# Performance work log

Measured on AMD Instinct MI355X. Metric: run time of the kernel, lower is better.

## Reference

```python
import jax, jax.numpy as jnp
import numpy as np

D_MODEL = 1024
NUM_HEADS = 16
HEAD_DIM = D_MODEL // NUM_HEADS
FFN_HIDDEN = 4096
EPS = 1e-5


def setup_inputs() -> dict:
    key = jax.random.key(0)
    ks = jax.random.split(key, 7)
    s = 0.02
    return {
        "x": jax.random.normal(ks[0], (2, 2048, D_MODEL), dtype=jnp.float32),
        "W_qkv": jax.random.normal(ks[1], (D_MODEL, 3 * D_MODEL), dtype=jnp.float32) * s,
        "b_qkv": jnp.zeros((3 * D_MODEL,), dtype=jnp.float32),
        "W_o": jax.random.normal(ks[2], (D_MODEL, D_MODEL), dtype=jnp.float32) * s,
        "b_o": jnp.zeros((D_MODEL,), dtype=jnp.float32),
        "gamma1": jnp.ones((D_MODEL,), dtype=jnp.float32),
        "beta1": jnp.zeros((D_MODEL,), dtype=jnp.float32),
        "W1": jax.random.normal(ks[3], (D_MODEL, FFN_HIDDEN), dtype=jnp.float32) * s,
        "b1": jnp.zeros((FFN_HIDDEN,), dtype=jnp.float32),
        "W2": jax.random.normal(ks[4], (FFN_HIDDEN, D_MODEL), dtype=jnp.float32) * s,
        "b2": jnp.zeros((D_MODEL,), dtype=jnp.float32),
        "gamma2": jnp.ones((D_MODEL,), dtype=jnp.float32),
        "beta2": jnp.zeros((D_MODEL,), dtype=jnp.float32),
    }


def _layernorm(x, gamma, beta):
    mean = jnp.mean(x, axis=-1, keepdims=True)
    var = jnp.mean((x - mean) ** 2, axis=-1, keepdims=True)
    return gamma * (x - mean) / jnp.sqrt(var + EPS) + beta


def reference(x, W_qkv, b_qkv, W_o, b_o, gamma1, beta1, W1, b1, W2, b2, gamma2, beta2):
    B, S, D = x.shape
    # ---- multi-head attention ----
    qkv = x @ W_qkv + b_qkv                       # [B,S,3D]
    qkv = qkv.reshape(B, S, NUM_HEADS, 3 * HEAD_DIM).transpose(0, 2, 1, 3)  # [B,H,S,3hd]
    q, k, v = jnp.split(qkv, 3, axis=-1)          # each [B,H,S,hd]
    scores = jnp.einsum("bhqd,bhkd->bhqk", q, k) / np.sqrt(HEAD_DIM)
    attn = jax.nn.softmax(scores, axis=-1)
    vals = jnp.einsum("bhqk,bhkd->bhqd", attn, v)
    vals = vals.transpose(0, 2, 1, 3).reshape(B, S, D)
    attn_out = vals @ W_o + b_o
    # dropout disabled (eval mode)
    h = _layernorm(attn_out + x, gamma1, beta1)
    # ---- position-wise FFN (dropout before relu per source, disabled) ----
    ffn = jax.nn.relu(h @ W1 + b1) @ W2 + b2
    return _layernorm(ffn + h, gamma2, beta2)
```

## Files before the change

### kernel.cpp

```cpp
#include <hip/hip_runtime.h>
#include <stdint.h>

typedef float v4f __attribute__((ext_vector_type(4)));
typedef __bf16 v8bf __attribute__((ext_vector_type(8)));
typedef __bf16 v4bf __attribute__((ext_vector_type(4)));
typedef unsigned short v8us __attribute__((ext_vector_type(8)));
typedef unsigned short v4us __attribute__((ext_vector_type(4)));

__device__ __forceinline__ float b2f(unsigned short u) {
    union { float f; uint32_t i; } x; x.i = ((uint32_t)u) << 16; return x.f;
}
__device__ __forceinline__ unsigned short f2b(float f) {
    union { float f; uint32_t u; } x; x.f = f;
    uint32_t r = x.u + 0x7fffu + ((x.u >> 16) & 1u);
    return (unsigned short)(r >> 16);
}

__global__ __launch_bounds__(256) void convert_f32_bf16(
    const float* __restrict__ src, unsigned short* __restrict__ dst)
{
    int i = (blockIdx.x * 256 + threadIdx.x) * 4;
    float4 v = *(const float4*)&src[i];
    v4us o = {f2b(v.x), f2b(v.y), f2b(v.z), f2b(v.w)};
    *(v4us*)&dst[i] = o;
}

__global__ __launch_bounds__(256) void transpose_to_bt(
    const float* __restrict__ W, unsigned short* __restrict__ WT, int K, int N)
{
    __shared__ unsigned short t[64][65];
    const int kb = blockIdx.y * 64, nb = blockIdx.x * 64;
    const int r = threadIdx.x >> 4, c4 = (threadIdx.x & 15) * 4;
    #pragma unroll
    for (int i = 0; i < 4; ++i) {
        int k = r + i * 16;
        float4 v = *(const float4*)&W[(size_t)(kb + k) * N + nb + c4];
        t[c4 + 0][k] = f2b(v.x);
        t[c4 + 1][k] = f2b(v.y);
        t[c4 + 2][k] = f2b(v.z);
        t[c4 + 3][k] = f2b(v.w);
    }
    __syncthreads();
    #pragma unroll
    for (int i = 0; i < 4; ++i) {
        int n = r + i * 16;
        v4us o = {t[n][c4], t[n][c4 + 1], t[n][c4 + 2], t[n][c4 + 3]};
        *(v4us*)&WT[(size_t)(nb + n) * K + kb + c4] = o;
    }
}

__device__ __forceinline__ void xcd_swizzle(int& bm, int& bn) {
    int NB = gridDim.x, MB = gridDim.y;
    int flat = blockIdx.x + NB * blockIdx.y;
    int xcd = flat & 7, j = flat >> 3;
    int MBand = MB >> 3;
    bm = xcd * MBand + (j % MBand);
    bn = j / MBand;
}

template<int SPLIT_V>
__global__ __launch_bounds__(256) void gemm_bt(
    const unsigned short* __restrict__ A, const unsigned short* __restrict__ BT,
    const float* __restrict__ bias, unsigned short* __restrict__ C,
    unsigned short* __restrict__ VT, int M, int N, int K, int relu)
{
    __shared__ __align__(16) unsigned short sA[2][128 * 32];
    __shared__ __align__(16) unsigned short sB[2][128 * 32];
    const int tid  = threadIdx.x;
    const int wave = tid >> 6, lane = tid & 63;
    const int wm = wave >> 1, wn = wave & 1;
    const int quad = lane >> 4, l16 = lane & 15;
    int bm, bn;
    xcd_swizzle(bm, bn);

    const int srow = lane >> 2, scol = (lane & 3) * 8;
    const unsigned short* ga0 = A  + (size_t)(bm * 128 + (wave * 2 + 0) * 16 + srow) * K + scol;
    const unsigned short* ga1 = A  + (size_t)(bm * 128 + (wave * 2 + 1) * 16 + srow) * K + scol;
    const unsigned short* gb0 = BT + (size_t)(bn * 128 + (wave * 2 + 0) * 16 + srow) * K + scol;
    const unsigned short* gb1 = BT + (size_t)(bn * 128 + (wave * 2 + 1) * 16 + srow) * K + scol;
    const int o0 = (wave * 2 + 0) * 512 + lane * 8;
    const int o1 = (wave * 2 + 1) * 512 + lane * 8;

    v8us aR[2][2], bR[2][2];
    #pragma unroll
    for (int c = 0; c < 2; ++c) {
        aR[c][0] = *(const v8us*)(ga0 + c * 32);
        aR[c][1] = *(const v8us*)(ga1 + c * 32);
        bR[c][0] = *(const v8us*)(gb0 + c * 32);
        bR[c][1] = *(const v8us*)(gb1 + c * 32);
    }

    v4f acc[4][4];
    #pragma unroll
    for (int i = 0; i < 4; ++i)
        #pragma unroll
        for (int j = 0; j < 4; ++j)
            acc[i][j] = (v4f){0.f, 0.f, 0.f, 0.f};

    for (int kt = 0; kt < K; kt += 64) {
        __syncthreads();
        #pragma unroll
        for (int c = 0; c < 2; ++c) {
            *(v8us*)&sA[c][o0] = aR[c][0];
            *(v8us*)&sA[c][o1] = aR[c][1];
            *(v8us*)&sB[c][o0] = bR[c][0];
            *(v8us*)&sB[c][o1] = bR[c][1];
        }
        __syncthreads();
        if (kt + 64 < K) {
            int kn = kt + 64;
            #pragma unroll
            for (int c = 0; c < 2; ++c) {
                aR[c][0] = *(const v8us*)(ga0 + kn + c * 32);
                aR[c][1] = *(const v8us*)(ga1 + kn + c * 32);
                bR[c][0] = *(const v8us*)(gb0 + kn + c * 32);
                bR[c][1] = *(const v8us*)(gb1 + kn + c * 32);
            }
        }

        #pragma unroll
        for (int c = 0; c < 2; ++c) {
            v8bf af[4], bfr[4];
            #pragma unroll
            for (int mt = 0; mt < 4; ++mt)
                af[mt] = *(const v8bf*)&sA[c][(wm * 64 + mt * 16 + l16) * 32 + quad * 8];
            #pragma unroll
            for (int nt = 0; nt < 4; ++nt)
                bfr[nt] = *(const v8bf*)&sB[c][(wn * 64 + nt * 16 + l16) * 32 + quad * 8];
            #pragma unroll
            for (int mt = 0; mt < 4; ++mt)
                #pragma unroll
                for (int nt = 0; nt < 4; ++nt)
                    acc[mt][nt] = __builtin_amdgcn_mfma_f32_16x16x32_bf16(
                        af[mt], bfr[nt], acc[mt][nt], 0, 0, 0);
        }
    }

    #pragma unroll
    for (int mt = 0; mt < 4; ++mt) {
        int row = bm * 128 + wm * 64 + mt * 16 + quad * 4;
        #pragma unroll
        for (int nt = 0; nt < 4; ++nt) {
            int c0 = bn * 128 + wn * 64 + nt * 16;
            int col = c0 + l16;
            float bv = bias ? bias[col] : 0.f;
            if (SPLIT_V && (c0 % 192) >= 128) {
                int hh = c0 / 192;
                int d  = (c0 % 192) - 128 + l16;
                int bb = row >> 11;
                int s  = row & 2047;
                v4us st;
                #pragma unroll
                for (int r = 0; r < 4; ++r)
                    st[r] = f2b(acc[mt][nt][r] + bv);
                *(v4us*)&VT[((size_t)(bb * 16 + hh) * 64 + d) * 2048 + s] = st;
            } else {
                float qs = (SPLIT_V && (c0 % 192) < 64) ? 0.18033688f : 1.0f;
                #pragma unroll
                for (int r = 0; r < 4; ++r) {
                    float v = (acc[mt][nt][r] + bv) * qs;
                    if (relu) v = fmaxf(v, 0.f);
                    C[(size_t)(row + r) * N + col] = f2b(v);
                }
            }
        }
    }
}

__global__ __launch_bounds__(256) void gemm_bt_n64(
    const unsigned short* __restrict__ A, const unsigned short* __restrict__ BT,
    const float* __restrict__ bias, unsigned short* __restrict__ C,
    int M, int N, int K, int relu)
{
    __shared__ __align__(16) unsigned short sA[2][128 * 32];
    __shared__ __align__(16) unsigned short sB[2][64 * 32];
    const int tid  = threadIdx.x;
    const int wave = tid >> 6, lane = tid & 63;
    const int wm = wave >> 1, wn = wave & 1;
    const int quad = lane >> 4, l16 = lane & 15;
    int bm, bn;
    xcd_swizzle(bm, bn);

    const int srow = lane >> 2, scol = (lane & 3) * 8;
    const unsigned short* ga0 = A  + (size_t)(bm * 128 + (wave * 2 + 0) * 16 + srow) * K + scol;
    const unsigned short* ga1 = A  + (size_t)(bm * 128 + (wave * 2 + 1) * 16 + srow) * K + scol;
    const unsigned short* gb0 = BT + (size_t)(bn * 64 + wave * 16 + srow) * K + scol;
    const int oa0 = (wave * 2 + 0) * 512 + lane * 8;
    const int oa1 = (wave * 2 + 1) * 512 + lane * 8;
    const int ob  = wave * 512 + lane * 8;

    v8us aR[2][2], bR[2];
    #pragma unroll
    for (int c = 0; c < 2; ++c) {
        aR[c][0] = *(const v8us*)(ga0 + c * 32);
        aR[c][1] = *(const v8us*)(ga1 + c * 32);
        bR[c]    = *(const v8us*)(gb0 + c * 32);
    }

    v4f acc[4][2];
    #pragma unroll
    for (int i = 0; i < 4; ++i)
        #pragma unroll
        for (int j = 0; j < 2; ++j)
            acc[i][j] = (v4f){0.f, 0.f, 0.f, 0.f};

    for (int kt = 0; kt < K; kt += 64) {
        __syncthreads();
        #pragma unroll
        for (int c = 0; c < 2; ++c) {
            *(v8us*)&sA[c][oa0] = aR[c][0];
            *(v8us*)&sA[c][oa1] = aR[c][1];
            *(v8us*)&sB[c][ob]  = bR[c];
        }
        __syncthreads();
        if (kt + 64 < K) {
            int kn = kt + 64;
            #pragma unroll
            for (int c = 0; c < 2; ++c) {
                aR[c][0] = *(const v8us*)(ga0 + kn + c * 32);
                aR[c][1] = *(const v8us*)(ga1 + kn + c * 32);
                bR[c]    = *(const v8us*)(gb0 + kn + c * 32);
            }
        }

        #pragma unroll
        for (int c = 0; c < 2; ++c) {
            v8bf af[4], bfr[2];
            #pragma unroll
            for (int mt = 0; mt < 4; ++mt)
                af[mt] = *(const v8bf*)&sA[c][(wm * 64 + mt * 16 + l16) * 32 + quad * 8];
            #pragma unroll
            for (int nt = 0; nt < 2; ++nt)
                bfr[nt] = *(const v8bf*)&sB[c][(wn * 32 + nt * 16 + l16) * 32 + quad * 8];
            #pragma unroll
            for (int mt = 0; mt < 4; ++mt)
                #pragma unroll
                for (int nt = 0; nt < 2; ++nt)
                    acc[mt][nt] = __builtin_amdgcn_mfma_f32_16x16x32_bf16(
                        af[mt], bfr[nt], acc[mt][nt], 0, 0, 0);
        }
    }

    #pragma unroll
    for (int mt = 0; mt < 4; ++mt) {
        #pragma unroll
        for (int nt = 0; nt < 2; ++nt) {
            int col = bn * 64 + wn * 32 + nt * 16 + l16;
            float bv = bias ? bias[col] : 0.f;
            #pragma unroll
            for (int r = 0; r < 4; ++r) {
                int row = bm * 128 + wm * 64 + mt * 16 + quad * 4 + r;
                float v = acc[mt][nt][r] + bv;
                if (relu) v = fmaxf(v, 0.f);
                C[(size_t)row * N + col] = f2b(v);
            }
        }
    }
}

__global__ __launch_bounds__(256) void attn_mfma(
    const unsigned short* __restrict__ qkv, const unsigned short* __restrict__ VT,
    unsigned short* __restrict__ av)
{
    __shared__ __align__(16) unsigned short sK[64 * 72];
    __shared__ __align__(16) unsigned short sVT[64 * 72];
    __shared__ __align__(16) unsigned short sP[4][32 * 72];
    const int tid  = threadIdx.x;
    const int wave = tid >> 6, lane = tid & 63;
    const int quad = lane >> 4, l16 = lane & 15;
    const int blk = blockIdx.x;
    const int xcd = blk & 7, local = blk >> 3;
    const int bh = xcd * 4 + (local & 3);
    const int qb = local >> 2;
    const int h = bh & 15, b = bh >> 4;
    const int row0 = b * 2048;
    const int qbase = row0 + qb * 128 + wave * 32;
    const size_t qoff = (size_t)h * 192;
    const size_t koff = qoff + 64;

    v8bf qf[2][2];
    #pragma unroll
    for (int qt = 0; qt < 2; ++qt)
        #pragma unroll
        for (int kc = 0; kc < 2; ++kc)
            qf[qt][kc] = *(const v8bf*)&qkv[(size_t)(qbase + qt * 16 + l16) * 3072
                                            + qoff + kc * 32 + quad * 8];

    v4f o[4][2];
    #pragma unroll
    for (int dt = 0; dt < 4; ++dt)
        #pragma unroll
        for (int qt = 0; qt < 2; ++qt)
            o[dt][qt] = (v4f){0.f, 0.f, 0.f, 0.f};
    float ll[2] = {0.f, 0.f};

    const int k_key0 = tid >> 3,        k_oct = (tid & 7) * 8;
    const int k_key1 = (tid + 256) >> 3;
    const int v_d0 = tid >> 3,          v_koct = (tid & 7) * 8;
    const int v_d1 = (tid + 256) >> 3;
    const unsigned short* gK0 = qkv + (size_t)(row0 + k_key0) * 3072 + koff + k_oct;
    const unsigned short* gK1 = qkv + (size_t)(row0 + k_key1) * 3072 + koff + k_oct;
    const unsigned short* gV0 = VT + ((size_t)bh * 64 + v_d0) * 2048 + v_koct;
    const unsigned short* gV1 = VT + ((size_t)bh * 64 + v_d1) * 2048 + v_koct;
    const size_t stepK = (size_t)64 * 3072;
    const size_t stepV = 64;

    v8us kreg0 = *(const v8us*)gK0, kreg1 = *(const v8us*)gK1;
    v8us vreg0 = *(const v8us*)gV0, vreg1 = *(const v8us*)gV1;
    gK0 += stepK; gK1 += stepK; gV0 += stepV; gV1 += stepV;

    for (int kt = 0; kt < 32; ++kt) {
        __syncthreads();
        *(v8us*)&sK[k_key0 * 72 + k_oct] = kreg0;
        *(v8us*)&sK[k_key1 * 72 + k_oct] = kreg1;
        *(v8us*)&sVT[v_d0 * 72 + v_koct] = vreg0;
        *(v8us*)&sVT[v_d1 * 72 + v_koct] = vreg1;
        __syncthreads();
        if (kt < 31) {
            kreg0 = *(const v8us*)gK0; kreg1 = *(const v8us*)gK1;
            vreg0 = *(const v8us*)gV0; vreg1 = *(const v8us*)gV1;
            gK0 += stepK; gK1 += stepK; gV0 += stepV; gV1 += stepV;
        }

        v4f sc[4][2];
        #pragma unroll
        for (int kk = 0; kk < 4; ++kk) {
            #pragma unroll
            for (int qt = 0; qt < 2; ++qt)
                sc[kk][qt] = (v4f){0.f, 0.f, 0.f, 0.f};
            #pragma unroll
            for (int kc = 0; kc < 2; ++kc) {
                v8bf ak = *(const v8bf*)&sK[(kk * 16 + l16) * 72 + kc * 32 + quad * 8];
                #pragma unroll
                for (int qt = 0; qt < 2; ++qt)
                    sc[kk][qt] = __builtin_amdgcn_mfma_f32_16x16x32_bf16(
                        ak, qf[qt][kc], sc[kk][qt], 0, 0, 0);
            }
        }

        #pragma unroll
        for (int qt = 0; qt < 2; ++qt) {
            float ps = 0.f;
            #pragma unroll
            for (int kk = 0; kk < 4; ++kk) {
                v4bf pk;
                #pragma unroll
                for (int rr = 0; rr < 4; ++rr) {
                    float p = __builtin_amdgcn_exp2f(sc[kk][qt][rr]);
                    ps += p;
                    pk[rr] = (__bf16)p;
                }
                *(v4bf*)&sP[wave][(qt * 16 + l16) * 72 + kk * 16 + quad * 4] = pk;
            }
            ll[qt] += ps;
        }

        __asm__ volatile("s_waitcnt lgkmcnt(0)" ::: "memory");

        #pragma unroll
        for (int c = 0; c < 2; ++c) {
            v8bf pb[2];
            #pragma unroll
            for (int qt = 0; qt < 2; ++qt) {
                union { v8bf v; v8us u; } u;
                u.u = *(const v8us*)&sP[wave][(qt * 16 + l16) * 72 + c * 32 + quad * 8];
                pb[qt] = u.v;
            }
            #pragma unroll
            for (int dt = 0; dt < 4; ++dt) {
                v8bf va = *(const v8bf*)&sVT[(dt * 16 + l16) * 72 + c * 32 + quad * 8];
                #pragma unroll
                for (int qt = 0; qt < 2; ++qt)
                    o[dt][qt] = __builtin_amdgcn_mfma_f32_16x16x32_bf16(
                        va, pb[qt], o[dt][qt], 0, 0, 0);
            }
        }
    }

    #pragma unroll
    for (int qt = 0; qt < 2; ++qt) {
        float l = ll[qt];
        l += __shfl_xor(l, 16, 64);
        l += __shfl_xor(l, 32, 64);
        float inv = 1.f / l;
        int qrow = qbase + qt * 16 + l16;
        #pragma unroll
        for (int dt = 0; dt < 4; ++dt) {
            v4bf st;
            #pragma unroll
            for (int rr = 0; rr < 4; ++rr)
                st[rr] = (__bf16)(o[dt][qt][rr] * inv);
            *(v4bf*)&av[(size_t)qrow * 1024 + h * 64 + dt * 16 + quad * 4] = st;
        }
    }
}

template<int RES_F32, int OUT_F32>
__global__ __launch_bounds__(256) void ln_fused(
    const unsigned short* __restrict__ a, const void* __restrict__ residv,
    const float* __restrict__ gamma, const float* __restrict__ beta,
    void* __restrict__ outv)
{
    const int row = blockIdx.x, tid = threadIdx.x;
    const size_t base = (size_t)row * 1024;
    const int c0 = tid * 4;
    ushort4 avv = *(const ushort4*)&a[base + c0];
    float y[4];
    if (RES_F32) {
        float4 rv = *(const float4*)((const float*)residv + base + c0);
        y[0] = b2f(avv.x) + rv.x;
        y[1] = b2f(avv.y) + rv.y;
        y[2] = b2f(avv.z) + rv.z;
        y[3] = b2f(avv.w) + rv.w;
    } else {
        ushort4 rv = *(const ushort4*)((const unsigned short*)residv + base + c0);
        y[0] = b2f(avv.x) + b2f(rv.x);
        y[1] = b2f(avv.y) + b2f(rv.y);
        y[2] = b2f(avv.z) + b2f(rv.z);
        y[3] = b2f(avv.w) + b2f(rv.w);
    }
    float s  = y[0] + y[1] + y[2] + y[3];
    float ss = y[0]*y[0] + y[1]*y[1] + y[2]*y[2] + y[3]*y[3];
    #pragma unroll
    for (int off = 32; off; off >>= 1) {
        s  += __shfl_xor(s, off, 64);
        ss += __shfl_xor(ss, off, 64);
    }
    __shared__ float red[8];
    int wave = tid >> 6, lane = tid & 63;
    if (lane == 0) { red[wave] = s; red[4 + wave] = ss; }
    __syncthreads();
    s  = red[0] + red[1] + red[2] + red[3];
    ss = red[4] + red[5] + red[6] + red[7];
    float mean = s * (1.f / 1024.f);
    float var  = ss * (1.f / 1024.f) - mean * mean;
    float rstd = rsqrtf(var + 1e-5f);
    float4 gv = *(const float4*)&gamma[c0];
    float4 bv = *(const float4*)&beta[c0];
    float r0 = gv.x * (y[0] - mean) * rstd + bv.x;
    float r1 = gv.y * (y[1] - mean) * rstd + bv.y;
    float r2 = gv.z * (y[2] - mean) * rstd + bv.z;
    float r3 = gv.w * (y[3] - mean) * rstd + bv.w;
    if (OUT_F32) {
        float4 ov = {r0, r1, r2, r3};
        *(float4*)((float*)outv + base + c0) = ov;
    } else {
        ushort4 ov;
        ov.x = f2b(r0); ov.y = f2b(r1); ov.z = f2b(r2); ov.w = f2b(r3);
        *(ushort4*)((unsigned short*)outv + base + c0) = ov;
    }
}

extern "C" void kernel_launch(void* const* d_in, const int* in_sizes, int n_in,
                              void* d_out, int out_size, void* d_ws, size_t ws_size,
                              hipStream_t stream)
{
    (void)in_sizes; (void)n_in; (void)out_size; (void)ws_size;
    const float* x    = (const float*)d_in[0];
    const float* Wqkv = (const float*)d_in[1];
    const float* bqkv = (const float*)d_in[2];
    const float* Wo   = (const float*)d_in[3];
    const float* bo   = (const float*)d_in[4];
    const float* g1   = (const float*)d_in[5];
    const float* be1  = (const float*)d_in[6];
    const float* W1   = (const float*)d_in[7];
    const float* b1   = (const float*)d_in[8];
    const float* W2   = (const float*)d_in[9];
    const float* b2   = (const float*)d_in[10];
    const float* g2   = (const float*)d_in[11];
    const float* be2  = (const float*)d_in[12];
    float* out = (float*)d_out;

    unsigned short* R0 = (unsigned short*)d_ws;
    unsigned short* R1 = R0 + (size_t)16 * 1024 * 1024;
    unsigned short* R2 = R1 + (size_t)4 * 1024 * 1024;
    unsigned short* R3 = R2 + (size_t)4 * 1024 * 1024;
    unsigned short* WqkvT = R0 + (size_t)12 * 1024 * 1024;

    const int M = 4096;
    dim3 blk(256);

    convert_f32_bf16<<<dim3(M * 1024 / 1024), blk, 0, stream>>>(x, R2);
    transpose_to_bt<<<dim3(48, 16), blk, 0, stream>>>(Wqkv, WqkvT, 1024, 3072);
    gemm_bt<1><<<dim3(24, 32), blk, 0, stream>>>(R2, WqkvT, bqkv, R0, R1, M, 3072, 1024, 0);
    attn_mfma<<<dim3(512), blk, 0, stream>>>(R0, R1, R3);
    transpose_to_bt<<<dim3(16, 16), blk, 0, stream>>>(Wo, R2, 1024, 1024);
    gemm_bt_n64<<<dim3(16, 32), blk, 0, stream>>>(R3, R2, bo, R1, M, 1024, 1024, 0);
    ln_fused<1, 0><<<dim3(4096), blk, 0, stream>>>(R1, x, g1, be1, R2);
    transpose_to_bt<<<dim3(64, 16), blk, 0, stream>>>(W1, R3, 1024, 4096);
    gemm_bt<0><<<dim3(32, 32), blk, 0, stream>>>(R2, R3, b1, R0, nullptr, M, 4096, 1024, 1);
    transpose_to_bt<<<dim3(16, 64), blk, 0, stream>>>(W2, R1, 4096, 1024);
    gemm_bt_n64<<<dim3(16, 32), blk, 0, stream>>>(R0, R1, b2, R3, M, 1024, 4096, 0);
    ln_fused<0, 1><<<dim3(4096), blk, 0, stream>>>(R3, R2, g2, be2, out);
}
```

Measured before the change: 353.0 us.

## Use direct global-to-LDS loads in GEMMs and halve attention query tile

Both GEMM kernels now stage tiles with direct global-to-LDS loads (global_load_lds) instead of going through registers. gemm_bt_n64 becomes double-buffered, so the next tile loads while the current one computes. gemm_bt instead loads and consumes each tile synchronously, which drops its register prefetch overlap. The attention kernel gives each wave 16 query rows instead of 32 and launches twice as many blocks, trading K/V tile reuse for more parallelism and fewer registers.

```diff
diff --git a/kernel.cpp b/kernel.cpp
--- a/kernel.cpp
+++ b/kernel.cpp
@@ -14,6 +14,13 @@
     union { float f; uint32_t u; } x; x.f = f;
     uint32_t r = x.u + 0x7fffu + ((x.u >> 16) & 1u);
     return (unsigned short)(r >> 16);
+}
+
+__device__ __forceinline__ void gload16(const unsigned short* g, unsigned short* l) {
+    __builtin_amdgcn_global_load_lds(
+        (const __attribute__((address_space(1))) void*)g,
+        (__attribute__((address_space(3))) void*)l,
+        16, 0, 0);
 }
 
 __global__ __launch_bounds__(256) void convert_f32_bf16(
@@ -73,22 +80,9 @@
     int bm, bn;
     xcd_swizzle(bm, bn);
 
-    const int srow = lane >> 2, scol = (lane & 3) * 8;
-    const unsigned short* ga0 = A  + (size_t)(bm * 128 + (wave * 2 + 0) * 16 + srow) * K + scol;
-    const unsigned short* ga1 = A  + (size_t)(bm * 128 + (wave * 2 + 1) * 16 + srow) * K + scol;
-    const unsigned short* gb0 = BT + (size_t)(bn * 128 + (wave * 2 + 0) * 16 + srow) * K + scol;
-    const unsigned short* gb1 = BT + (size_t)(bn * 128 + (wave * 2 + 1) * 16 + srow) * K + scol;
-    const int o0 = (wave * 2 + 0) * 512 + lane * 8;
-    const int o1 = (wave * 2 + 1) * 512 + lane * 8;
-
-    v8us aR[2][2], bR[2][2];
-    #pragma unroll
-    for (int c = 0; c < 2; ++c) {
-        aR[c][0] = *(const v8us*)(ga0 + c * 32);
-        aR[c][1] = *(const v8us*)(ga1 + c * 32);
-        bR[c][0] = *(const v8us*)(gb0 + c * 32);
-        bR[c][1] = *(const v8us*)(gb1 + c * 32);
-    }
+    const int lrow = lane >> 2, lcol = (lane & 3) * 8;
+    const unsigned short* gA = A  + (size_t)(bm * 128) * K + lcol;
+    const unsigned short* gB = BT + (size_t)(bn * 128) * K + lcol;
 
     v4f acc[4][4];
     #pragma unroll
@@ -101,22 +95,14 @@
         __syncthreads();
         #pragma unroll
         for (int c = 0; c < 2; ++c) {
-            *(v8us*)&sA[c][o0] = aR[c][0];
-            *(v8us*)&sA[c][o1] = aR[c][1];
-            *(v8us*)&sB[c][o0] = bR[c][0];
-            *(v8us*)&sB[c][o1] = bR[c][1];
+            #pragma unroll
+            for (int j = 0; j < 2; ++j) {
+                const int r0 = wave * 32 + j * 16;
+                gload16(gA + (size_t)(r0 + lrow) * K + kt + c * 32, &sA[c][r0 * 32]);
+                gload16(gB + (size_t)(r0 + lrow) * K + kt + c * 32, &sB[c][r0 * 32]);
+            }
         }
         __syncthreads();
-        if (kt + 64 < K) {
-            int kn = kt + 64;
-            #pragma unroll
-            for (int c = 0; c < 2; ++c) {
-                aR[c][0] = *(const v8us*)(ga0 + kn + c * 32);
-                aR[c][1] = *(const v8us*)(ga1 + kn + c * 32);
-                bR[c][0] = *(const v8us*)(gb0 + kn + c * 32);
-                bR[c][1] = *(const v8us*)(gb1 + kn + c * 32);
-            }
-        }
 
         #pragma unroll
         for (int c = 0; c < 2; ++c) {
@@ -172,8 +158,8 @@
     const float* __restrict__ bias, unsigned short* __restrict__ C,
     int M, int N, int K, int relu)
 {
-    __shared__ __align__(16) unsigned short sA[2][128 * 32];
-    __shared__ __align__(16) unsigned short sB[2][64 * 32];
+    __shared__ __align__(16) unsigned short sA[2][2][128 * 32];
+    __shared__ __align__(16) unsigned short sB[2][2][64 * 32];
     const int tid  = threadIdx.x;
     const int wave = tid >> 6, lane = tid & 63;
     const int wm = wave >> 1, wn = wave & 1;
@@ -181,21 +167,22 @@
     int bm, bn;
     xcd_swizzle(bm, bn);
 
-    const int srow = lane >> 2, scol = (lane & 3) * 8;
-    const unsigned short* ga0 = A  + (size_t)(bm * 128 + (wave * 2 + 0) * 16 + srow) * K + scol;
-    const unsigned short* ga1 = A  + (size_t)(bm * 128 + (wave * 2 + 1) * 16 + srow) * K + scol;
-    const unsigned short* gb0 = BT + (size_t)(bn * 64 + wave * 16 + srow) * K + scol;
-    const int oa0 = (wave * 2 + 0) * 512 + lane * 8;
-    const int oa1 = (wave * 2 + 1) * 512 + lane * 8;
-    const int ob  = wave * 512 + lane * 8;
-
-    v8us aR[2][2], bR[2];
-    #pragma unroll
-    for (int c = 0; c < 2; ++c) {
-        aR[c][0] = *(const v8us*)(ga0 + c * 32);
-        aR[c][1] = *(const v8us*)(ga1 + c * 32);
-        bR[c]    = *(const v8us*)(gb0 + c * 32);
-    }
+    const int lrow = lane >> 2, lcol = (lane & 3) * 8;
+    const unsigned short* gA = A  + (size_t)(bm * 128) * K + lcol;
+    const unsigned short* gB = BT + (size_t)(bn * 64) * K + lcol;
+
+    auto stage = [&](int buf, int kt0) {
+        #pragma unroll
+        for (int c = 0; c < 2; ++c) {
+            #pragma unroll
+            for (int j = 0; j < 2; ++j) {
+                const int r0 = wave * 32 + j * 16;
+                gload16(gA + (size_t)(r0 + lrow) * K + kt0 + c * 32, &sA[buf][c][r0 * 32]);
+            }
+            const int r0b = wave * 16;
+            gload16(gB + (size_t)(r0b + lrow) * K + kt0 + c * 32, &sB[buf][c][r0b * 32]);
+        }
+    };
 
     v4f acc[4][2];
     #pragma unroll
@@ -204,34 +191,21 @@
         for (int j = 0; j < 2; ++j)
             acc[i][j] = (v4f){0.f, 0.f, 0.f, 0.f};
 
+    stage(0, 0);
+    __syncthreads();
+    int cur = 0;
     for (int kt = 0; kt < K; kt += 64) {
-        __syncthreads();
-        #pragma unroll
-        for (int c = 0; c < 2; ++c) {
-            *(v8us*)&sA[c][oa0] = aR[c][0];
-            *(v8us*)&sA[c][oa1] = aR[c][1];
-            *(v8us*)&sB[c][ob]  = bR[c];
-        }
-        __syncthreads();
-        if (kt + 64 < K) {
-            int kn = kt + 64;
-            #pragma unroll
-            for (int c = 0; c < 2; ++c) {
-                aR[c][0] = *(const v8us*)(ga0 + kn + c * 32);
-                aR[c][1] = *(const v8us*)(ga1 + kn + c * 32);
-                bR[c]    = *(const v8us*)(gb0 + kn + c * 32);
-            }
-        }
+        if (kt + 64 < K) stage(cur ^ 1, kt + 64);
 
         #pragma unroll
         for (int c = 0; c < 2; ++c) {
             v8bf af[4], bfr[2];
             #pragma unroll
             for (int mt = 0; mt < 4; ++mt)
-                af[mt] = *(const v8bf*)&sA[c][(wm * 64 + mt * 16 + l16) * 32 + quad * 8];
+                af[mt] = *(const v8bf*)&sA[cur][c][(wm * 64 + mt * 16 + l16) * 32 + quad * 8];
             #pragma unroll
             for (int nt = 0; nt < 2; ++nt)
-                bfr[nt] = *(const v8bf*)&sB[c][(wn * 32 + nt * 16 + l16) * 32 + quad * 8];
+                bfr[nt] = *(const v8bf*)&sB[cur][c][(wn * 32 + nt * 16 + l16) * 32 + quad * 8];
             #pragma unroll
             for (int mt = 0; mt < 4; ++mt)
                 #pragma unroll
@@ -239,6 +213,8 @@
                     acc[mt][nt] = __builtin_amdgcn_mfma_f32_16x16x32_bf16(
                         af[mt], bfr[nt], acc[mt][nt], 0, 0, 0);
         }
+        __syncthreads();
+        cur ^= 1;
     }
 
     #pragma unroll
@@ -264,7 +240,7 @@
 {
     __shared__ __align__(16) unsigned short sK[64 * 72];
     __shared__ __align__(16) unsigned short sVT[64 * 72];
-    __shared__ __align__(16) unsigned short sP[4][32 * 72];
+    __shared__ __align__(16) unsigned short sP[4][16 * 72];
     const int tid  = threadIdx.x;
     const int wave = tid >> 6, lane = tid & 63;
     const int quad = lane >> 4, l16 = lane & 15;
@@ -274,25 +250,21 @@
     const int qb = local >> 2;
     const int h = bh & 15, b = bh >> 4;
     const int row0 = b * 2048;
-    const int qbase = row0 + qb * 128 + wave * 32;
+    const int qbase = row0 + qb * 64 + wave * 16;
     const size_t qoff = (size_t)h * 192;
     const size_t koff = qoff + 64;
 
-    v8bf qf[2][2];
-    #pragma unroll
-    for (int qt = 0; qt < 2; ++qt)
-        #pragma unroll
-        for (int kc = 0; kc < 2; ++kc)
-            qf[qt][kc] = *(const v8bf*)&qkv[(size_t)(qbase + qt * 16 + l16) * 3072
-                                            + qoff + kc * 32 + quad * 8];
-
-    v4f o[4][2];
+    v8bf qf[2];
+    #pragma unroll
+    for (int kc = 0; kc < 2; ++kc)
+        qf[kc] = *(const v8bf*)&qkv[(size_t)(qbase + l16) * 3072
+                                    + qoff + kc * 32 + quad * 8];
+
+    v4f o[4];
     #pragma unroll
     for (int dt = 0; dt < 4; ++dt)
-        #pragma unroll
-        for (int qt = 0; qt < 2; ++qt)
-            o[dt][qt] = (v4f){0.f, 0.f, 0.f, 0.f};
-    float ll[2] = {0.f, 0.f};
+        o[dt] = (v4f){0.f, 0.f, 0.f, 0.f};
+    float ll = 0.f;
 
     const int k_key0 = tid >> 3,        k_oct = (tid & 7) * 8;
     const int k_key1 = (tid + 256) >> 3;
@@ -322,76 +294,60 @@
             gK0 += stepK; gK1 += stepK; gV0 += stepV; gV1 += stepV;
         }
 
-        v4f sc[4][2];
+        v4f sc[4];
         #pragma unroll
         for (int kk = 0; kk < 4; ++kk) {
-            #pragma unroll
-            for (int qt = 0; qt < 2; ++qt)
-                sc[kk][qt] = (v4f){0.f, 0.f, 0.f, 0.f};
+            sc[kk] = (v4f){0.f, 0.f, 0.f, 0.f};
             #pragma unroll
             for (int kc = 0; kc < 2; ++kc) {
                 v8bf ak = *(const v8bf*)&sK[(kk * 16 + l16) * 72 + kc * 32 + quad * 8];
-                #pragma unroll
-                for (int qt = 0; qt < 2; ++qt)
-                    sc[kk][qt] = __builtin_amdgcn_mfma_f32_16x16x32_bf16(
-                        ak, qf[qt][kc], sc[kk][qt], 0, 0, 0);
-            }
-        }
-
-        #pragma unroll
-        for (int qt = 0; qt < 2; ++qt) {
-            float ps = 0.f;
-            #pragma unroll
-            for (int kk = 0; kk < 4; ++kk) {
-                v4bf pk;
-                #pragma unroll
-                for (int rr = 0; rr < 4; ++rr) {
-                    float p = __builtin_amdgcn_exp2f(sc[kk][qt][rr]);
-                    ps += p;
-                    pk[rr] = (__bf16)p;
-                }
-                *(v4bf*)&sP[wave][(qt * 16 + l16) * 72 + kk * 16 + quad * 4] = pk;
-            }
-            ll[qt] += ps;
-        }
+                sc[kk] = __builtin_amdgcn_mfma_f32_16x16x32_bf16(
+                    ak, qf[kc], sc[kk], 0, 0, 0);
+            }
+        }
+
+        float ps = 0.f;
+        #pragma unroll
+        for (int kk = 0; kk < 4; ++kk) {
+            v4bf pk;
+            #pragma unroll
+            for (int rr = 0; rr < 4; ++rr) {
+                float p = __builtin_amdgcn_exp2f(sc[kk][rr]);
+                ps += p;
+                pk[rr] = (__bf16)p;
+            }
+            *(v4bf*)&sP[wave][l16 * 72 + kk * 16 + quad * 4] = pk;
+        }
+        ll += ps;
 
         __asm__ volatile("s_waitcnt lgkmcnt(0)" ::: "memory");
 
         #pragma unroll
         for (int c = 0; c < 2; ++c) {
-            v8bf pb[2];
-            #pragma unroll
-            for (int qt = 0; qt < 2; ++qt) {
-                union { v8bf v; v8us u; } u;
-                u.u = *(const v8us*)&sP[wave][(qt * 16 + l16) * 72 + c * 32 + quad * 8];
-                pb[qt] = u.v;
-            }
+            union { v8bf v; v8us u; } u;
+            u.u = *(const v8us*)&sP[wave][l16 * 72 + c * 32 + quad * 8];
+            v8bf pb = u.v;
             #pragma unroll
             for (int dt = 0; dt < 4; ++dt) {
                 v8bf va = *(const v8bf*)&sVT[(dt * 16 + l16) * 72 + c * 32 + quad * 8];
-                #pragma unroll
-                for (int qt = 0; qt < 2; ++qt)
-                    o[dt][qt] = __builtin_amdgcn_mfma_f32_16x16x32_bf16(
-                        va, pb[qt], o[dt][qt], 0, 0, 0);
-            }
-        }
-    }
-
-    #pragma unroll
-    for (int qt = 0; qt < 2; ++qt) {
-        float l = ll[qt];
-        l += __shfl_xor(l, 16, 64);
-        l += __shfl_xor(l, 32, 64);
-        float inv = 1.f / l;
-        int qrow = qbase + qt * 16 + l16;
-        #pragma unroll
-        for (int dt = 0; dt < 4; ++dt) {
-            v4bf st;
-            #pragma unroll
-            for (int rr = 0; rr < 4; ++rr)
-                st[rr] = (__bf16)(o[dt][qt][rr] * inv);
-            *(v4bf*)&av[(size_t)qrow * 1024 + h * 64 + dt * 16 + quad * 4] = st;
-        }
+                o[dt] = __builtin_amdgcn_mfma_f32_16x16x32_bf16(
+                    va, pb, o[dt], 0, 0, 0);
+            }
+        }
+    }
+
+    float l = ll;
+    l += __shfl_xor(l, 16, 64);
+    l += __shfl_xor(l, 32, 64);
+    float inv = 1.f / l;
+    int qrow = qbase + l16;
+    #pragma unroll
+    for (int dt = 0; dt < 4; ++dt) {
+        v4bf st;
+        #pragma unroll
+        for (int rr = 0; rr < 4; ++rr)
+            st[rr] = (__bf16)(o[dt][rr] * inv);
+        *(v4bf*)&av[(size_t)qrow * 1024 + h * 64 + dt * 16 + quad * 4] = st;
     }
 }
 
@@ -483,7 +439,7 @@
     convert_f32_bf16<<<dim3(M * 1024 / 1024), blk, 0, stream>>>(x, R2);
     transpose_to_bt<<<dim3(48, 16), blk, 0, stream>>>(Wqkv, WqkvT, 1024, 3072);
     gemm_bt<1><<<dim3(24, 32), blk, 0, stream>>>(R2, WqkvT, bqkv, R0, R1, M, 3072, 1024, 0);
-    attn_mfma<<<dim3(512), blk, 0, stream>>>(R0, R1, R3);
+    attn_mfma<<<dim3(1024), blk, 0, stream>>>(R0, R1, R3);
     transpose_to_bt<<<dim3(16, 16), blk, 0, stream>>>(Wo, R2, 1024, 1024);
     gemm_bt_n64<<<dim3(16, 32), blk, 0, stream>>>(R3, R2, bo, R1, M, 1024, 1024, 0);
     ln_fused<1, 0><<<dim3(4096), blk, 0, stream>>>(R1, x, g1, be1, R2);
```

Result: slower. 380.2 us (+7.7%).

## Add 256x256-tile double-buffered GEMM with direct global-to-LDS loads for FFN1

Applied to the files above, without the earlier changes.

Replaces the FFN first-layer GEMM (4096x4096x1024 with bias and ReLU) with a new 512-thread kernel that computes 256x256 output tiles. Operand tiles are staged through double-buffered LDS filled by global_load_lds, with an XOR swizzle to reduce bank conflicts. The larger tile raises arithmetic intensity and cuts global traffic per FLOP. In exchange the grid drops to 256 blocks, which lowers occupancy and tail balance, and each thread holds 128 accumulator registers.

```diff
diff --git a/kernel.cpp b/kernel.cpp
--- a/kernel.cpp
+++ b/kernel.cpp
@@ -14,6 +14,13 @@
     union { float f; uint32_t u; } x; x.f = f;
     uint32_t r = x.u + 0x7fffu + ((x.u >> 16) & 1u);
     return (unsigned short)(r >> 16);
+}
+
+__device__ __forceinline__ void gload16(const unsigned short* g, unsigned short* l) {
+    __builtin_amdgcn_global_load_lds(
+        (const __attribute__((address_space(1))) void*)g,
+        (__attribute__((address_space(3))) void*)l,
+        16, 0, 0);
 }
 
 __global__ __launch_bounds__(256) void convert_f32_bf16(
@@ -253,6 +260,106 @@
                 float v = acc[mt][nt][r] + bv;
                 if (relu) v = fmaxf(v, 0.f);
                 C[(size_t)row * N + col] = f2b(v);
+            }
+        }
+    }
+}
+
+__global__ __launch_bounds__(512) void gemm256(
+    const unsigned short* __restrict__ A, const unsigned short* __restrict__ BT,
+    const float* __restrict__ bias, unsigned short* __restrict__ C,
+    int M, int N, int K, int relu)
+{
+    __shared__ __align__(16) unsigned short sA[2][256 * 64];
+    __shared__ __align__(16) unsigned short sB[2][256 * 64];
+    const int tid  = threadIdx.x;
+    const int wave = tid >> 6, lane = tid & 63;
+    const int wm = wave >> 2, wn = wave & 3;
+    const int quad = lane >> 4, l16 = lane & 15;
+    int bm, bn;
+    xcd_swizzle(bm, bn);
+
+    const int srow = lane >> 3;
+    const int scol = ((lane & 7) * 8) ^ ((lane & 32) ? 16 : 0);
+    size_t aoff[4], boff[4];
+    #pragma unroll
+    for (int j = 0; j < 4; ++j) {
+        int r = wave * 32 + j * 8 + srow;
+        aoff[j] = (size_t)(bm * 256 + r) * K + scol;
+        boff[j] = (size_t)(bn * 256 + r) * K + scol;
+    }
+    const int lds0 = wave * 32 * 64;
+
+    const int ksw = (quad * 8) ^ ((l16 & 4) ? 16 : 0);
+
+    v4f acc[8][4];
+    #pragma unroll
+    for (int i = 0; i < 8; ++i)
+        #pragma unroll
+        for (int j = 0; j < 4; ++j)
+            acc[i][j] = (v4f){0.f, 0.f, 0.f, 0.f};
+
+    const int NT = K >> 6;
+    #pragma unroll
+    for (int j = 0; j < 4; ++j) {
+        gload16(A  + aoff[j], &sA[0][lds0 + j * 512]);
+        gload16(BT + boff[j], &sB[0][lds0 + j * 512]);
+    }
+    __syncthreads();
+
+    for (int t = 0; t < NT; ++t) {
+        const int buf = t & 1;
+        if (t + 1 < NT) {
+            const int ktn = (t + 1) << 6;
+            #pragma unroll
+            for (int j = 0; j < 4; ++j) {
+                gload16(A  + aoff[j] + ktn, &sA[buf ^ 1][lds0 + j * 512]);
+                gload16(BT + boff[j] + ktn, &sB[buf ^ 1][lds0 + j * 512]);
+            }
+        }
+
+        v8bf bfr[4][2];
+        #pragma unroll
+        for (int nt2 = 0; nt2 < 4; ++nt2)
+            #pragma unroll
+            for (int kc = 0; kc < 2; ++kc)
+                bfr[nt2][kc] = *(const v8bf*)&sB[buf][
+                    (wn * 64 + nt2 * 16 + l16) * 64 + kc * 32 + ksw];
+        #pragma unroll
+        for (int mq = 0; mq < 2; ++mq) {
+            v8bf af[4][2];
+            #pragma unroll
+            for (int mt2 = 0; mt2 < 4; ++mt2)
+                #pragma unroll
+                for (int kc = 0; kc < 2; ++kc)
+                    af[mt2][kc] = *(const v8bf*)&sA[buf][
+                        (wm * 128 + mq * 64 + mt2 * 16 + l16) * 64 + kc * 32 + ksw];
+            #pragma unroll
+            for (int mt2 = 0; mt2 < 4; ++mt2)
+                #pragma unroll
+                for (int nt2 = 0; nt2 < 4; ++nt2)
+                    #pragma unroll
+                    for (int kc = 0; kc < 2; ++kc)
+                        acc[mq * 4 + mt2][nt2] =
+                            __builtin_amdgcn_mfma_f32_16x16x32_bf16(
+                                af[mt2][kc], bfr[nt2][kc],
+                                acc[mq * 4 + mt2][nt2], 0, 0, 0);
+        }
+        __syncthreads();
+    }
+
+    #pragma unroll
+    for (int mt = 0; mt < 8; ++mt) {
+        int row = bm * 256 + wm * 128 + mt * 16 + quad * 4;
+        #pragma unroll
+        for (int nt = 0; nt < 4; ++nt) {
+            int col = bn * 256 + wn * 64 + nt * 16 + l16;
+            float bv = bias ? bias[col] : 0.f;
+            #pragma unroll
+            for (int r = 0; r < 4; ++r) {
+                float v = acc[mt][nt][r] + bv;
+                if (relu) v = fmaxf(v, 0.f);
+                C[(size_t)(row + r) * N + col] = f2b(v);
             }
         }
     }
@@ -488,7 +595,7 @@
     gemm_bt_n64<<<dim3(16, 32), blk, 0, stream>>>(R3, R2, bo, R1, M, 1024, 1024, 0);
     ln_fused<1, 0><<<dim3(4096), blk, 0, stream>>>(R1, x, g1, be1, R2);
     transpose_to_bt<<<dim3(64, 16), blk, 0, stream>>>(W1, R3, 1024, 4096);
-    gemm_bt<0><<<dim3(32, 32), blk, 0, stream>>>(R2, R3, b1, R0, nullptr, M, 4096, 1024, 1);
+    gemm256<<<dim3(16, 16), dim3(512), 0, stream>>>(R2, R3, b1, R0, M, 4096, 1024, 1);
     transpose_to_bt<<<dim3(16, 64), blk, 0, stream>>>(W2, R1, 4096, 1024);
     gemm_bt_n64<<<dim3(16, 32), blk, 0, stream>>>(R0, R1, b2, R3, M, 1024, 4096, 0);
     ln_fused<0, 1><<<dim3(4096), blk, 0, stream>>>(R3, R2, g2, be2, out);
```

Result: no change. 347.0 us (-1.7%).
